# Kernel tuning notes

Hardware: AMD Instinct MI355X
Metric: run time of the kernel (lower is better)

Reference implementation:

```python
import jax, jax.numpy as jnp
import numpy as np

B = 1024
N_NODES = 30
E_PER = 82
IN_F = 128
HID = 256
HEADS = (3, 2, 1)
N_EH = 41


def _lin(k, fi, fo):
    s = 1.0 / np.sqrt(fi)
    kw, kb = jax.random.split(k)
    W = jax.random.uniform(kw, (fi, fo), jnp.float32, -s, s)
    b = jax.random.uniform(kb, (fo,), jnp.float32, -s, s)
    return W, b


def setup_inputs() -> dict:
    key = jax.random.key(0)
    ks = list(jax.random.split(key, 32))
    rng = np.random.default_rng(0)
    # base 30-node graph with E_PER directed edges, no self-loops
    src = rng.integers(0, N_NODES, E_PER)
    dst = (src + rng.integers(1, N_NODES, E_PER)) % N_NODES
    base = np.stack([src, dst])  # [2, E_PER]
    offs = (np.arange(B) * N_NODES)[None, None, :]  # [1,1,B]
    ei = (base[:, :, None] + offs).transpose(0, 2, 1).reshape(2, -1)  # [2, B*E_PER]
    e_h = rng.choice(E_PER, N_EH, replace=False)
    d = {}
    d["x"] = jax.random.normal(ks[0], (B * N_NODES, IN_F), jnp.float32)
    d["edge_index"] = jnp.asarray(ei, dtype=jnp.int32)
    d["e_h_pairs"] = jnp.asarray(base[:, e_h].T, dtype=jnp.int32)  # [N_EH, 2]
    d["Wp"], d["bp"] = _lin(ks[1], IN_F, HID)
    i = 2
    for l, H in enumerate(HEADS):
        d[f"ln_g{l}"] = jnp.ones((HID,), jnp.float32)
        d[f"ln_b{l}"] = jnp.zeros((HID,), jnp.float32)
        d[f"Wl{l}"], d[f"bl{l}"] = _lin(ks[i], HID, H * HID); i += 1
        d[f"Wr{l}"], d[f"br{l}"] = _lin(ks[i], HID, H * HID); i += 1
        d[f"att{l}"] = jax.random.normal(ks[i], (H, HID), jnp.float32) * 0.1; i += 1
        d[f"bias{l}"] = jnp.zeros((HID,), jnp.float32)
    dims = [2 * HID, 256, 128, 128, 1]
    for j in range(4):
        d[f"Wm{j}"], d[f"bm{j}"] = _lin(ks[i], dims[j], dims[j + 1]); i += 1
    return d


def _layer_norm(h, g, b):
    mu = jnp.mean(h, -1, keepdims=True)
    var = jnp.mean((h - mu) ** 2, -1, keepdims=True)
    return (h - mu) * jax.lax.rsqrt(var + 1e-5) * g + b


def _gatv2(h, src, dst, n, Wl, bl, Wr, br, att, bias):
    # PyG GATv2Conv, concat=False (mean over heads), self-loops already in src/dst
    H, C = att.shape
    xl = (h @ Wl + bl).reshape(-1, H, C)  # source transform
    xr = (h @ Wr + br).reshape(-1, H, C)  # target transform
    xj = xl[src]                          # [E,H,C]
    e = jax.nn.leaky_relu(xj + xr[dst], 0.2)
    logits = jnp.einsum('ehc,hc->eh', e, att)  # [E,H]
    m = jax.lax.stop_gradient(jax.ops.segment_max(logits, dst, num_segments=n))
    ex = jnp.exp(logits - m[dst])
    denom = jax.ops.segment_sum(ex, dst, num_segments=n)
    alpha = ex / denom[dst]               # softmax over incoming edges of dst
    out = jax.ops.segment_sum(xj * alpha[..., None], dst, num_segments=n)  # [N,H,C]
    return jnp.mean(out, 1) + bias


def reference(x, edge_index, e_h_pairs, Wp, bp,
              ln_g0, ln_b0, Wl0, bl0, Wr0, br0, att0, bias0,
              ln_g1, ln_b1, Wl1, bl1, Wr1, br1, att1, bias1,
              ln_g2, ln_b2, Wl2, bl2, Wr2, br2, att2, bias2,
              Wm0, bm0, Wm1, bm1, Wm2, bm2, Wm3, bm3):
    n = x.shape[0]
    loops = jnp.arange(n, dtype=edge_index.dtype)
    src = jnp.concatenate([edge_index[0], loops])
    dst = jnp.concatenate([edge_index[1], loops])
    lrelu = lambda v: jax.nn.leaky_relu(v, 0.01)
    h = x @ Wp + bp
    layers = [(ln_g0, ln_b0, Wl0, bl0, Wr0, br0, att0, bias0),
              (ln_g1, ln_b1, Wl1, bl1, Wr1, br1, att1, bias1),
              (ln_g2, ln_b2, Wl2, bl2, Wr2, br2, att2, bias2)]
    for (g, b, Wl, bl, Wr, br, att, bias) in layers:
        hn = _layer_norm(h, g, b)
        hc = _gatv2(hn, src, dst, n, Wl, bl, Wr, br, att, bias)
        h = lrelu(hc) + h  # dropout is identity in eval
    hb = h.reshape(-1, N_NODES, HID)  # [B, 30, 256]
    ef = jnp.concatenate([hb[:, e_h_pairs[:, 0], :], hb[:, e_h_pairs[:, 1], :]], -1)
    o = ef.reshape(-1, 2 * HID)
    o = lrelu(o @ Wm0 + bm0)
    o = lrelu(o @ Wm1 + bm1)
    o = lrelu(o @ Wm2 + bm2)
    o = o @ Wm3 + bm3
    return o.reshape(-1)
```

## Files before the change

kernel.cpp:

```cpp
#include <hip/hip_runtime.h>
#include <hip/hip_bf16.h>
#include <math.h>

#define N_NODES 30
#define E_BASE  82
#define E_TOT   112
#define B_GRAPH 1024
#define HID     256
#define NTOT    (B_GRAPH * N_NODES)
#define MAXIN   32
#define N_EH    41
#define M_MLP   (B_GRAPH * N_EH)

#define META_SRC  0
#define META_DST  E_TOT
#define META_CNT  (2 * E_TOT)
#define META_LIST 256
#define META_INTS 1216

typedef __attribute__((ext_vector_type(8))) short bf16x8;
typedef __attribute__((ext_vector_type(4))) short bf16x4;
typedef __attribute__((ext_vector_type(4))) float f32x4;
#define AS3 __attribute__((address_space(3)))
#define AS1 __attribute__((address_space(1)))
// ... 25 lines not shown
      if (tid < E_BASE) { s = ei[tid]; d = ei[B_GRAPH * E_BASE + tid]; }
      else              { s = tid - E_BASE; d = s; }
      meta[META_SRC + tid] = s;
      meta[META_DST + tid] = d;
      int pos = atomicAdd(&cnt[d], 1);
      if (pos < MAXIN) meta[META_LIST + d * MAXIN + pos] = tid;
    }
    __syncthreads();
    if (tid < N_NODES) meta[META_CNT + tid] = cnt[tid];
    return;
  }
  int ji = 0;
  #pragma unroll
  for (int i = 1; i < 10; i++) if (b >= args.j[i].tstart) ji = i;
  WtJob jb = args.j[ji];
  int t = b - jb.tstart;
  int ntn = jb.N >> 5;
  int tk = t / ntn, tn = t - tk * ntn;
  int k0 = tk * 32, n0 = tn * 32;
  __shared__ float s[32][33];
  int tx = threadIdx.x & 31, ty = threadIdx.x >> 5;
  #pragma unroll
  for (int p = 0; p < 4; p++)
    s[ty + p * 8][tx] = jb.in[(size_t)(k0 + ty + p * 8) * jb.N + n0 + tx];
  __syncthreads();
  __hip_bfloat16* o = out + jb.ooff;
  #pragma unroll
  for (int p = 0; p < 4; p++) {
    int n = ty + p * 8;
    o[(size_t)(n0 + n) * jb.K + k0 + tx] = __float2bfloat16(s[tx][n]);
  }
}

template<int ACT, int OUTBF>
__global__ __launch_bounds__(256)
void gemm_mfma(const __hip_bfloat16* __restrict__ A, const __hip_bfloat16* __restrict__ Bt,
               const float* __restrict__ bias, const float* __restrict__ bias2,
               void* __restrict__ Cv, int M, int K, int N, int N1)
{
  __shared__ __hip_bfloat16 sA[2][128 * 32];
  __shared__ __hip_bfloat16 sB[2][128 * 32];
  const int tid = threadIdx.x;
  const int lane = tid & 63;
  const int wave = tid >> 6;
  const int wx = wave & 1, wy = wave >> 1;
  const int bm = blockIdx.x, bn = blockIdx.y;
  const int mrow = lane & 15, quad = lane >> 4;

  const int r0 = tid >> 2, kc0 = (tid & 3) * 8;
  const __hip_bfloat16* Ag0 = A + (size_t)(bm * 128 + r0) * K + kc0;
  const __hip_bfloat16* Ag1 = A + (size_t)(bm * 128 + r0 + 64) * K + kc0;
  const __hip_bfloat16* Bg0 = Bt + (size_t)(bn * 128 + r0) * K + kc0;
  const __hip_bfloat16* Bg1 = Bt + (size_t)(bn * 128 + r0 + 64) * K + kc0;

  f32x4 acc[4][4];
  #pragma unroll
  for (int i = 0; i < 4; i++)
    #pragma unroll
    for (int j = 0; j < 4; j++)
      acc[i][j] = (f32x4){0.f, 0.f, 0.f, 0.f};

  for (int kt = 0; kt < K; kt += 64) {
    __syncthreads();
    #pragma unroll
    for (int s = 0; s < 2; s++) {
      gload_lds16(Ag0 + kt + s * 32, &sA[s][tid * 8]);
      gload_lds16(Ag1 + kt + s * 32, &sA[s][2048 + tid * 8]);
      gload_lds16(Bg0 + kt + s * 32, &sB[s][tid * 8]);
      gload_lds16(Bg1 + kt + s * 32, &sB[s][2048 + tid * 8]);
    }
    __syncthreads();

    #pragma unroll
    for (int s = 0; s < 2; s++) {
      bf16x8 af[4], bfr[4];
      #pragma unroll
      for (int i = 0; i < 4; i++) {
        af[i]  = *(const bf16x8*)&sA[s][(wy * 64 + i * 16 + mrow) * 32 + quad * 8];
        bfr[i] = *(const bf16x8*)&sB[s][(wx * 64 + i * 16 + mrow) * 32 + quad * 8];
      }
      #pragma unroll
      for (int i = 0; i < 4; i++)
        #pragma unroll
        for (int j = 0; j < 4; j++)
          acc[i][j] = __builtin_amdgcn_mfma_f32_16x16x32_bf16(af[i], bfr[j], acc[i][j], 0, 0, 0);
    }
  }

  #pragma unroll
  for (int i = 0; i < 4; i++) {
    #pragma unroll
    for (int r = 0; r < 4; r++) {
      size_t row = (size_t)bm * 128 + wy * 64 + i * 16 + quad * 4 + r;
      #pragma unroll
      for (int j = 0; j < 4; j++) {
        int col = bn * 128 + wx * 64 + j * 16 + mrow;
        float bc = (col < N1) ? bias[col] : bias2[col - N1];
        float v = acc[i][j][r] + bc;
        if (ACT) v = v > 0.f ? v : 0.01f * v;
        if (OUTBF) ((__hip_bfloat16*)Cv)[row * N + col] = __float2bfloat16(v);
        else       ((float*)Cv)[row * N + col] = v;
      }
    }
  }
}

template<int ACT, int OUTBF>
__global__ __launch_bounds__(256)
void gemm_mfma_f32a(const float* __restrict__ A, const __hip_bfloat16* __restrict__ Bt,
                    const float* __restrict__ bias, void* __restrict__ Cv,
                    int M, int K, int N)
{
  __shared__ __hip_bfloat16 sA[128 * 32];
  __shared__ __hip_bfloat16 sB[128 * 32];
  const int tid = threadIdx.x;
  const int lane = tid & 63;
  const int wave = tid >> 6;
  const int wx = wave & 1, wy = wave >> 1;
  const int bm = blockIdx.x, bn = blockIdx.y;
  const int mrow = lane & 15, quad = lane >> 4;

  const int r0 = tid >> 2, kc0 = (tid & 3) * 8;
  const float* Ag0 = A + (size_t)(bm * 128 + r0) * K + kc0;
  const float* Ag1 = A + (size_t)(bm * 128 + r0 + 64) * K + kc0;
  const __hip_bfloat16* Bg0 = Bt + (size_t)(bn * 128 + r0) * K + kc0;
  const __hip_bfloat16* Bg1 = Bt + (size_t)(bn * 128 + r0 + 64) * K + kc0;

  f32x4 acc[4][4];
  #pragma unroll
  for (int i = 0; i < 4; i++)
    #pragma unroll
    for (int j = 0; j < 4; j++)
      acc[i][j] = (f32x4){0.f, 0.f, 0.f, 0.f};

// ... 58 lines not shown
  const int K = 512;
  __shared__ __hip_bfloat16 sA[128 * 32];
  __shared__ __hip_bfloat16 sB[128 * 32];
  const int tid = threadIdx.x;
  const int lane = tid & 63;
  const int wave = tid >> 6;
  const int wx = wave & 1, wy = wave >> 1;
  const int bm = blockIdx.x, bn = blockIdx.y;
  const int mrow = lane & 15, quad = lane >> 4;

  const float* pu[2]; const float* pv[2]; int sub[2];
  #pragma unroll
  for (int cI = 0; cI < 2; cI++) {
    int c = tid + cI * 256;
    int r0 = c >> 2; sub[cI] = (c & 3) * 8;
    int R = bm * 128 + r0;
    int b = R / N_EH, p = R - b * N_EH;
    int u = pairs[p * 2], v = pairs[p * 2 + 1];
    pu[cI] = h + ((size_t)b * N_NODES + u) * HID;
    pv[cI] = h + ((size_t)b * N_NODES + v) * HID;
  }

  const int r0 = tid >> 2, kc0 = (tid & 3) * 8;
  const __hip_bfloat16* Bg0 = Bt + (size_t)(bn * 128 + r0) * K + kc0;
  const __hip_bfloat16* Bg1 = Bt + (size_t)(bn * 128 + r0 + 64) * K + kc0;

  f32x4 acc[4][4];
  #pragma unroll
  for (int i = 0; i < 4; i++)
    #pragma unroll
    for (int j = 0; j < 4; j++)
      acc[i][j] = (f32x4){0.f, 0.f, 0.f, 0.f};

  for (int kt = 0; kt < K; kt += 32) {
    float4 av[2][2];
    #pragma unroll
    for (int cI = 0; cI < 2; cI++) {
      const float* src = (kt < 256 ? pu[cI] + kt : pv[cI] + kt - 256) + sub[cI];
      av[cI][0] = *(const float4*)src;
      av[cI][1] = *(const float4*)(src + 4);
    }
    __syncthreads();
    #pragma unroll
    for (int cI = 0; cI < 2; cI++) {
      __hip_bfloat16 t[8];
      t[0] = __float2bfloat16(av[cI][0].x); t[1] = __float2bfloat16(av[cI][0].y);
      t[2] = __float2bfloat16(av[cI][0].z); t[3] = __float2bfloat16(av[cI][0].w);
      t[4] = __float2bfloat16(av[cI][1].x); t[5] = __float2bfloat16(av[cI][1].y);
      t[6] = __float2bfloat16(av[cI][1].z); t[7] = __float2bfloat16(av[cI][1].w);
      *(bf16x8*)&sA[(tid + cI * 256) * 8] = *(bf16x8*)t;
    }
    gload_lds16(Bg0 + kt, &sB[tid * 8]);
    gload_lds16(Bg1 + kt, &sB[2048 + tid * 8]);
    __syncthreads();

    bf16x8 af[4], bfr[4];
    #pragma unroll
    for (int i = 0; i < 4; i++) {
      af[i]  = *(const bf16x8*)&sA[(wy * 64 + i * 16 + mrow) * 32 + quad * 8];
      bfr[i] = *(const bf16x8*)&sB[(wx * 64 + i * 16 + mrow) * 32 + quad * 8];
    }
    #pragma unroll
    for (int i = 0; i < 4; i++)
      #pragma unroll
      for (int j = 0; j < 4; j++)
        acc[i][j] = __builtin_amdgcn_mfma_f32_16x16x32_bf16(af[i], bfr[j], acc[i][j], 0, 0, 0);
  }
// ... 134 lines not shown
      }
    }
  }
  __syncthreads();
  if (tid < 128)
    out[(size_t)bm * 128 + tid] = spart[0][tid] + spart[1][tid] + b3[0];
}

__global__ __launch_bounds__(256)
void layernorm(const float* __restrict__ h, const float* __restrict__ g,
               const float* __restrict__ b, __hip_bfloat16* __restrict__ hn)
{
  const int wv = threadIdx.x >> 6, lane = threadIdx.x & 63;
  const size_t row = (size_t)blockIdx.x * 4 + wv;
  const float* hr = h + row * HID;
  float v[4];
  float sum = 0.f;
  #pragma unroll
  for (int j = 0; j < 4; j++) { v[j] = hr[lane + 64 * j]; sum += v[j]; }
  #pragma unroll
  for (int off = 32; off; off >>= 1) sum += __shfl_xor(sum, off);
  float mu = sum * (1.f / 256.f);
  float vs = 0.f;
  #pragma unroll
  for (int j = 0; j < 4; j++) { float d = v[j] - mu; vs += d * d; }
  #pragma unroll
  for (int off = 32; off; off >>= 1) vs += __shfl_xor(vs, off);
  float rs = rsqrtf(vs * (1.f / 256.f) + 1e-5f);
  __hip_bfloat16* outr = hn + row * HID;
  #pragma unroll
  for (int j = 0; j < 4; j++) {
    int c = lane + 64 * j;
    outr[c] = __float2bfloat16((v[j] - mu) * rs * g[c] + b[c]);
  }
}

__global__ __launch_bounds__(256)
void gat_alpha(const __hip_bfloat16* __restrict__ xcat,
               const float* __restrict__ att, float* __restrict__ alphaG,
               const int* __restrict__ meta, int H)
{
  __shared__ __hip_bfloat16 sxl[N_NODES * HID];
  __shared__ __hip_bfloat16 sxr[N_NODES * HID];
  __shared__ float slog[E_TOT];
  __shared__ float smax[N_NODES];
  __shared__ float sden[N_NODES];
  __shared__ int ssrc[E_TOT], sdst[E_TOT], scnt[N_NODES], slist[N_NODES * MAXIN];

  const int tid = threadIdx.x;
  const int g = blockIdx.x, hh = blockIdx.y;
  const size_t nodebase = (size_t)g * N_NODES;
  const int S = 2 * H * HID;

  {
    int i = tid;
    #pragma unroll
    for (int p = 0; p < 4; p++, i += 256) {
      if (i < N_NODES * HID / 8) {
        int node = i >> 5, c = (i & 31) * 8;
        const __hip_bfloat16* row = &xcat[(nodebase + node) * S + c];
        gload_lds16(row + hh * HID, &sxl[(size_t)i * 8]);
        gload_lds16(row + (H + hh) * HID, &sxr[(size_t)i * 8]);
      }
    }
  }

  if (tid < E_TOT) { ssrc[tid] = meta[META_SRC + tid]; sdst[tid] = meta[META_DST + tid]; }
  if (tid < N_NODES) { scnt[tid] = meta[META_CNT + tid]; sden[tid] = 0.f; }
  for (int i = tid; i < N_NODES * MAXIN; i += 256) slist[i] = meta[META_LIST + i];

  const int wv = tid >> 6, l32 = tid & 31, esub = (tid >> 5) & 1;
  const int c0 = l32 * 8;
  float attr[8];
  #pragma unroll
  for (int j = 0; j < 8; j++) attr[j] = att[hh * HID + c0 + j];
  __syncthreads();

  #pragma unroll
  for (int pass = 0; pass < 14; pass++) {
    int e = pass * 8 + wv * 2 + esub;
    bf16x8 a = *(const bf16x8*)&sxl[ssrc[e] * HID + c0];
    bf16x8 b = *(const bf16x8*)&sxr[sdst[e] * HID + c0];
    float sum = 0.f;
    #pragma unroll
    for (int j = 0; j < 8; j++) {
      float v = b2f(a[j]) + b2f(b[j]);
      v = v > 0.f ? v : 0.2f * v;
      sum += v * attr[j];
    }
    #pragma unroll
    for (int off = 16; off; off >>= 1) sum += __shfl_xor(sum, off);
    if (l32 == 0) slog[e] = sum;
  }
  __syncthreads();

  if (tid < N_NODES) {
    int cnt = scnt[tid];
    const int* lst = &slist[tid * MAXIN];
    float m = -1e30f;
    for (int i = 0; i < cnt; i++) m = fmaxf(m, slog[lst[i]]);
    smax[tid] = m;
  }
  __syncthreads();
  if (tid < E_TOT) {
    float ex = expf(slog[tid] - smax[sdst[tid]]);
    slog[tid] = ex;
    atomicAdd(&sden[sdst[tid]], ex);
  }
  __syncthreads();
  if (tid < E_TOT)
    alphaG[((size_t)g * H + hh) * E_TOT + tid] = slog[tid] / sden[sdst[tid]];
}

template<int DO_LN>
__global__ __launch_bounds__(256, 4)
void gat_agg(const __hip_bfloat16* __restrict__ xcat, const float* __restrict__ alphaG,
             const float* __restrict__ bias, float* __restrict__ h,
             const float* __restrict__ lnG, const float* __restrict__ lnB,
             __hip_bfloat16* __restrict__ hn, const int* __restrict__ meta, int H)
{
  __shared__ __hip_bfloat16 sxl[2][N_NODES * HID];
  __shared__ float salpha[2][E_TOT];
  __shared__ int ssrc[E_TOT], scnt[N_NODES], slist[N_NODES * MAXIN];

  const int tid = threadIdx.x;
  const int g = blockIdx.x;
  const size_t nodebase = (size_t)g * N_NODES;
  const int S = 2 * H * HID;
  const int c4 = tid & 63;
  const int ng = tid >> 6;

  if (tid < E_TOT) ssrc[tid] = meta[META_SRC + tid];
  if (tid < N_NODES) scnt[tid] = meta[META_CNT + tid];
  for (int i = tid; i < N_NODES * MAXIN; i += 256) slist[i] = meta[META_LIST + i];

  float4 hres[8];
  #pragma unroll
  for (int ki = 0; ki < 8; ki++) {
    int k = ng + ki * 4;
    if (k < N_NODES) hres[ki] = *(const float4*)&h[(nodebase + k) * HID + c4 * 4];
  }

  {
    int i = tid;
    #pragma unroll
    for (int p = 0; p < 4; p++, i += 256) {
      if (i < N_NODES * HID / 8) {
        int node = i >> 5, c = (i & 31) * 8;
        gload_lds16(&xcat[(nodebase + node) * S + 0 * HID + c], &sxl[0][(size_t)i * 8]);
      }
    }
    if (tid < E_TOT) salpha[0][tid] = alphaG[((size_t)g * H + 0) * E_TOT + tid];
  }

  float acc[8][4];
  #pragma unroll
  for (int ki = 0; ki < 8; ki++)
    #pragma unroll
    for (int j = 0; j < 4; j++) acc[ki][j] = 0.f;

  for (int hh = 0; hh < H; hh++) {
    const int buf = hh & 1;
    __syncthreads();
    if (hh + 1 < H) {
      const int nb = buf ^ 1;
      int i = tid;
      #pragma unroll
      for (int p = 0; p < 4; p++, i += 256) {
        if (i < N_NODES * HID / 8) {
          int node = i >> 5, c = (i & 31) * 8;
          gload_lds16(&xcat[(nodebase + node) * S + (hh + 1) * HID + c], &sxl[nb][(size_t)i * 8]);
        }
      }
      if (tid < E_TOT) salpha[nb][tid] = alphaG[((size_t)g * H + hh + 1) * E_TOT + tid];
    }
    #pragma unroll
    for (int ki = 0; ki < 8; ki++) {
      int k = ng + ki * 4;
      if (k < N_NODES) {
        int cnt = scnt[k];
        const int* lst = &slist[k * MAXIN];
        for (int i = 0; i < cnt; i++) {
          int e = lst[i];
          float al = salpha[buf][e];
          bf16x4 v = *(const bf16x4*)&sxl[buf][ssrc[e] * HID + c4 * 4];
          acc[ki][0] += al * b2f(v[0]);
          acc[ki][1] += al * b2f(v[1]);
          acc[ki][2] += al * b2f(v[2]);
          acc[ki][3] += al * b2f(v[3]);
        }
      }
    }
  }

  const float invH = 1.f / (float)H;
  const float4 bs = *(const float4*)&bias[c4 * 4];
  float4 gv, bv;
  if (DO_LN) {
    gv = *(const float4*)&lnG[c4 * 4];
    bv = *(const float4*)&lnB[c4 * 4];
  }
  #pragma unroll
  for (int ki = 0; ki < 8; ki++) {
    int k = ng + ki * 4;
    if (k < N_NODES) {
      float o0 = acc[ki][0] * invH + bs.x; o0 = o0 > 0.f ? o0 : 0.01f * o0; o0 += hres[ki].x;
      float o1 = acc[ki][1] * invH + bs.y; o1 = o1 > 0.f ? o1 : 0.01f * o1; o1 += hres[ki].y;
      float o2 = acc[ki][2] * invH + bs.z; o2 = o2 > 0.f ? o2 : 0.01f * o2; o2 += hres[ki].z;
      float o3 = acc[ki][3] * invH + bs.w; o3 = o3 > 0.f ? o3 : 0.01f * o3; o3 += hres[ki].w;
      float4 o4 = {o0, o1, o2, o3};
      *(float4*)&h[(nodebase + k) * HID + c4 * 4] = o4;
      if (DO_LN) {
        float sum = o0 + o1 + o2 + o3;
        #pragma unroll
        for (int off = 32; off; off >>= 1) sum += __shfl_xor(sum, off);
        float mu = sum * (1.f / 256.f);
        float d0 = o0 - mu, d1 = o1 - mu, d2 = o2 - mu, d3 = o3 - mu;
        float vs = d0 * d0 + d1 * d1 + d2 * d2 + d3 * d3;
        #pragma unroll
        for (int off = 32; off; off >>= 1) vs += __shfl_xor(vs, off);
        float rs = rsqrtf(vs * (1.f / 256.f) + 1e-5f);
        __hip_bfloat16 t[4];
        t[0] = __float2bfloat16(d0 * rs * gv.x + bv.x);
        t[1] = __float2bfloat16(d1 * rs * gv.y + bv.y);
        t[2] = __float2bfloat16(d2 * rs * gv.z + bv.z);
        t[3] = __float2bfloat16(d3 * rs * gv.w + bv.w);
        *(bf16x4*)&hn[(nodebase + k) * HID + c4 * 4] = *(bf16x4*)t;
      }
    }
  }
}

extern "C" void kernel_launch(void* const* d_in, const int* in_sizes, int n_in,
                              void* d_out, int out_size, void* d_ws, size_t ws_size,
                              hipStream_t stream) {
  const float* x     = (const float*)d_in[0];
  const int*   ei    = (const int*)d_in[1];
  const int*   pairs = (const int*)d_in[2];
  const float* bp    = (const float*)d_in[4];
  const float *lng[3], *lnb[3], *bl[3], *br[3], *att[3], *bias[3];
  const float *WlF[3], *WrF[3];
  for (int l = 0; l < 3; l++) {
    int base = 5 + l * 8;
    lng[l]  = (const float*)d_in[base + 0];
    lnb[l]  = (const float*)d_in[base + 1];
    WlF[l]  = (const float*)d_in[base + 2];
    bl[l]   = (const float*)d_in[base + 3];
    WrF[l]  = (const float*)d_in[base + 4];
    br[l]   = (const float*)d_in[base + 5];
    att[l]  = (const float*)d_in[base + 6];
    bias[l] = (const float*)d_in[base + 7];
  }
  const float* WmF[4] = {(const float*)d_in[29], (const float*)d_in[31],
                         (const float*)d_in[33], (const float*)d_in[35]};
  const float* bm[4] = {(const float*)d_in[30], (const float*)d_in[32],
                        (const float*)d_in[34], (const float*)d_in[36]};

  float* ws  = (float*)d_ws;
  float* h   = ws;
  __hip_bfloat16* hnb = (__hip_bfloat16*)(ws + 7864320);
  __hip_bfloat16* xcat = (__hip_bfloat16*)(ws + 11796480);
  float* alphaG = ws + 35389440;
  __hip_bfloat16* wbuf = (__hip_bfloat16*)(ws + 35733504);
  int*   meta = (int*)(ws + 36233216);
  __hip_bfloat16* o1b = (__hip_bfloat16*)xcat;
  float* out = (float*)d_out;

  const int oWp = 0, oWl0 = 32768, oWr0 = 229376, oWl1 = 425984, oWr1 = 557056;
  const int oWl2 = 688128, oWr2 = 753664, oWm0 = 819200, oWm1 = 950272, oWm2 = 983040;

  WtArgs wa;
  wa.j[0] = {(const float*)d_in[3], 128, 256,   0, oWp };
  wa.j[1] = {WlF[0],              256, 768,  32, oWl0};
  wa.j[2] = {WrF[0],              256, 768, 224, oWr0};
  wa.j[3] = {WlF[1],              256, 512, 416, oWl1};
  wa.j[4] = {WrF[1],              256, 512, 544, oWr1};
  wa.j[5] = {WlF[2],              256, 256, 672, oWl2};
  wa.j[6] = {WrF[2],              256, 256, 736, oWr2};
  wa.j[7] = {WmF[0],              512, 256, 800, oWm0};
  wa.j[8] = {WmF[1],              256, 128, 928, oWm1};
  wa.j[9] = {WmF[2],              128, 128, 960, oWm2};
  transpose_weights<<<977, 256, 0, stream>>>(wa, wbuf, ei, meta);

  gemm_mfma_f32a<0, 0><<<dim3(NTOT / 128, 2), 256, 0, stream>>>(x, wbuf + oWp, bp, h,
                                                                NTOT, 128, 256);

  layernorm<<<NTOT / 4, 256, 0, stream>>>(h, lng[0], lnb[0], hnb);

  const int Hs[3] = {3, 2, 1};
  const int oWl[3] = {oWl0, oWl1, oWl2};
  for (int l = 0; l < 3; l++) {
    int N = 2 * Hs[l] * HID;
    gemm_mfma<0, 1><<<dim3(NTOT / 128, N / 128), 256, 0, stream>>>(
        hnb, wbuf + oWl[l], bl[l], br[l], xcat, NTOT, HID, N, N / 2);
    gat_alpha<<<dim3(B_GRAPH, Hs[l]), 256, 0, stream>>>(xcat, att[l], alphaG, meta, Hs[l]);
    if (l < 2)
      gat_agg<1><<<B_GRAPH, 256, 0, stream>>>(xcat, alphaG, bias[l], h,
                                              lng[l + 1], lnb[l + 1], hnb, meta, Hs[l]);
    else
      gat_agg<0><<<B_GRAPH, 256, 0, stream>>>(xcat, alphaG, bias[l], h,
                                              nullptr, nullptr, nullptr, meta, Hs[l]);
  }

  gemm_mfma_pair<<<dim3(M_MLP / 128, 2), 256, 0, stream>>>(h, pairs, wbuf + oWm0, bm[0], o1b, 256);
  mlp_tail<<<M_MLP / 128, 256, 0, stream>>>(o1b, wbuf + oWm1, bm[1], wbuf + oWm2, bm[2],
                                            WmF[3], bm[3], out);
}
```

Before: 437.5 us.

## Fuse GATv2 projection GEMM, attention and aggregation into one per-graph kernel

Replaces the per-layer sequence of projection GEMM, attention-logit kernel and aggregation kernel with a single kernel per layer, where each block owns one 30-node graph. The block computes the xl/xr projections with MFMA into shared memory and runs softmax and aggregation in place. This removes the large bf16 xcat intermediate and the alpha buffer round trips through global memory, and cuts launches from 9 to 3. In exchange, weights are read directly from global memory per block with no LDS tiling. The GEMM works on 32-row tiles padded from 30 rows, and the larger LDS footprint may lower occupancy.

```diff
diff --git a/kernel.cpp b/kernel.cpp
--- a/kernel.cpp
+++ b/kernel.cpp
@@ -81,74 +81,202 @@
   }
 }
 
-template<int ACT, int OUTBF>
+template<int DO_LN>
 __global__ __launch_bounds__(256)
-void gemm_mfma(const __hip_bfloat16* __restrict__ A, const __hip_bfloat16* __restrict__ Bt,
-               const float* __restrict__ bias, const float* __restrict__ bias2,
-               void* __restrict__ Cv, int M, int K, int N, int N1)
+void gat_fused(const __hip_bfloat16* hnb_io,
+               const __hip_bfloat16* __restrict__ Wl,
+               const __hip_bfloat16* __restrict__ Wr,
+               const float* __restrict__ blv, const float* __restrict__ brv,
+               const float* __restrict__ att, const float* __restrict__ bias,
+               float* __restrict__ h,
+               const float* __restrict__ lnG, const float* __restrict__ lnB,
+               const int* __restrict__ meta, int H)
 {
-  __shared__ __hip_bfloat16 sA[2][128 * 32];
-  __shared__ __hip_bfloat16 sB[2][128 * 32];
+  __shared__ __hip_bfloat16 sHn[8 * 32 * 32];
+  __shared__ __hip_bfloat16 sxl[N_NODES * HID];
+  __shared__ __hip_bfloat16 sxr[N_NODES * HID];
+  __shared__ float slog[E_TOT], salpha[E_TOT], smax[N_NODES], sden[N_NODES];
+  __shared__ int ssrc[E_TOT], sdst[E_TOT], scnt[N_NODES], slist[N_NODES * MAXIN];
+
   const int tid = threadIdx.x;
-  const int lane = tid & 63;
-  const int wave = tid >> 6;
-  const int wx = wave & 1, wy = wave >> 1;
-  const int bm = blockIdx.x, bn = blockIdx.y;
+  const int g = blockIdx.x;
+  const size_t nodebase = (size_t)g * N_NODES;
+  const int lane = tid & 63, wave = tid >> 6;
   const int mrow = lane & 15, quad = lane >> 4;
-
-  const int r0 = tid >> 2, kc0 = (tid & 3) * 8;
-  const __hip_bfloat16* Ag0 = A + (size_t)(bm * 128 + r0) * K + kc0;
-  const __hip_bfloat16* Ag1 = A + (size_t)(bm * 128 + r0 + 64) * K + kc0;
-  const __hip_bfloat16* Bg0 = Bt + (size_t)(bn * 128 + r0) * K + kc0;
-  const __hip_bfloat16* Bg1 = Bt + (size_t)(bn * 128 + r0 + 64) * K + kc0;
-
-  f32x4 acc[4][4];
-  #pragma unroll
-  for (int i = 0; i < 4; i++)
-    #pragma unroll
-    for (int j = 0; j < 4; j++)
-      acc[i][j] = (f32x4){0.f, 0.f, 0.f, 0.f};
-
-  for (int kt = 0; kt < K; kt += 64) {
-    __syncthreads();
-    #pragma unroll
-    for (int s = 0; s < 2; s++) {
-      gload_lds16(Ag0 + kt + s * 32, &sA[s][tid * 8]);
-      gload_lds16(Ag1 + kt + s * 32, &sA[s][2048 + tid * 8]);
-      gload_lds16(Bg0 + kt + s * 32, &sB[s][tid * 8]);
-      gload_lds16(Bg1 + kt + s * 32, &sB[s][2048 + tid * 8]);
-    }
-    __syncthreads();
-
-    #pragma unroll
-    for (int s = 0; s < 2; s++) {
-      bf16x8 af[4], bfr[4];
-      #pragma unroll
-      for (int i = 0; i < 4; i++) {
-        af[i]  = *(const bf16x8*)&sA[s][(wy * 64 + i * 16 + mrow) * 32 + quad * 8];
-        bfr[i] = *(const bf16x8*)&sB[s][(wx * 64 + i * 16 + mrow) * 32 + quad * 8];
-      }
-      #pragma unroll
-      for (int i = 0; i < 4; i++)
-        #pragma unroll
-        for (int j = 0; j < 4; j++)
-          acc[i][j] = __builtin_amdgcn_mfma_f32_16x16x32_bf16(af[i], bfr[j], acc[i][j], 0, 0, 0);
-    }
-  }
-
-  #pragma unroll
-  for (int i = 0; i < 4; i++) {
-    #pragma unroll
-    for (int r = 0; r < 4; r++) {
-      size_t row = (size_t)bm * 128 + wy * 64 + i * 16 + quad * 4 + r;
-      #pragma unroll
-      for (int j = 0; j < 4; j++) {
-        int col = bn * 128 + wx * 64 + j * 16 + mrow;
-        float bc = (col < N1) ? bias[col] : bias2[col - N1];
-        float v = acc[i][j][r] + bc;
-        if (ACT) v = v > 0.f ? v : 0.01f * v;
-        if (OUTBF) ((__hip_bfloat16*)Cv)[row * N + col] = __float2bfloat16(v);
-        else       ((float*)Cv)[row * N + col] = v;
+  const int n0 = wave * 64;
+  const int c4 = tid & 63, ng = tid >> 6;
+
+  {
+    const __hip_bfloat16* src = hnb_io + nodebase * HID;
+    #pragma unroll
+    for (int p = 0; p < 4; p++) {
+      int L = tid + p * 256;
+      int kk = L >> 7, rem = L & 127;
+      int row = rem >> 2, c16 = rem & 3;
+      if (row >= N_NODES) row = 0;
+      gload_lds16(src + (size_t)(row * 32 + kk * 4 + c16) * 8, &sHn[(size_t)L * 8]);
+    }
+  }
+  if (tid < E_TOT) { ssrc[tid] = meta[META_SRC + tid]; sdst[tid] = meta[META_DST + tid]; }
+  if (tid < N_NODES) scnt[tid] = meta[META_CNT + tid];
+  for (int i = tid; i < N_NODES * MAXIN; i += 256) slist[i] = meta[META_LIST + i];
+  __syncthreads();
+
+  float agg[8][4];
+  #pragma unroll
+  for (int ki = 0; ki < 8; ki++)
+    #pragma unroll
+    for (int j = 0; j < 4; j++) agg[ki][j] = 0.f;
+
+  for (int hh = 0; hh < H; hh++) {
+    for (int mat = 0; mat < 2; mat++) {
+      const __hip_bfloat16* W = (mat ? Wr : Wl) + ((size_t)hh * HID) * HID;
+      const float* bb = mat ? brv : blv;
+      __hip_bfloat16* sx = mat ? sxr : sxl;
+
+      f32x4 acc[2][4];
+      #pragma unroll
+      for (int mi = 0; mi < 2; mi++)
+        #pragma unroll
+        for (int nj = 0; nj < 4; nj++) acc[mi][nj] = (f32x4){0.f, 0.f, 0.f, 0.f};
+
+      #pragma unroll
+      for (int kk = 0; kk < 8; kk++) {
+        bf16x8 a0 = *(const bf16x8*)&sHn[kk * 1024 + mrow * 32 + quad * 8];
+        bf16x8 a1 = *(const bf16x8*)&sHn[kk * 1024 + (16 + mrow) * 32 + quad * 8];
+        bf16x8 bf[4];
+        #pragma unroll
+        for (int nj = 0; nj < 4; nj++)
+          bf[nj] = *(const bf16x8*)&W[(size_t)(n0 + nj * 16 + mrow) * HID + kk * 32 + quad * 8];
+        #pragma unroll
+        for (int nj = 0; nj < 4; nj++) {
+          acc[0][nj] = __builtin_amdgcn_mfma_f32_16x16x32_bf16(a0, bf[nj], acc[0][nj], 0, 0, 0);
+          acc[1][nj] = __builtin_amdgcn_mfma_f32_16x16x32_bf16(a1, bf[nj], acc[1][nj], 0, 0, 0);
+        }
+      }
+
+      if (mat == 0) __syncthreads();
+
+      float bv[4];
+      #pragma unroll
+      for (int nj = 0; nj < 4; nj++) bv[nj] = bb[hh * HID + n0 + nj * 16 + mrow];
+      #pragma unroll
+      for (int mi = 0; mi < 2; mi++) {
+        #pragma unroll
+        for (int r = 0; r < 4; r++) {
+          int row = mi * 16 + quad * 4 + r;
+          if (row < N_NODES) {
+            #pragma unroll
+            for (int nj = 0; nj < 4; nj++)
+              sx[row * HID + n0 + nj * 16 + mrow] = __float2bfloat16(acc[mi][nj][r] + bv[nj]);
+          }
+        }
+      }
+    }
+    __syncthreads();
+
+    {
+      const int l32 = tid & 31, esub = (tid >> 5) & 1;
+      const int c0 = l32 * 8;
+      float attr[8];
+      #pragma unroll
+      for (int j = 0; j < 8; j++) attr[j] = att[hh * HID + c0 + j];
+      if (tid < N_NODES) sden[tid] = 0.f;
+      #pragma unroll
+      for (int pass = 0; pass < 14; pass++) {
+        int e = pass * 8 + wave * 2 + esub;
+        bf16x8 a = *(const bf16x8*)&sxl[ssrc[e] * HID + c0];
+        bf16x8 b = *(const bf16x8*)&sxr[sdst[e] * HID + c0];
+        float sum = 0.f;
+        #pragma unroll
+        for (int j = 0; j < 8; j++) {
+          float v = b2f(a[j]) + b2f(b[j]);
+          v = v > 0.f ? v : 0.2f * v;
+          sum += v * attr[j];
+        }
+        #pragma unroll
+        for (int off = 16; off; off >>= 1) sum += __shfl_xor(sum, off);
+        if (l32 == 0) slog[e] = sum;
+      }
+    }
+    __syncthreads();
+
+    if (tid < N_NODES) {
+      int cnt = scnt[tid];
+      const int* lst = &slist[tid * MAXIN];
+      float m = -1e30f;
+      for (int i = 0; i < cnt; i++) m = fmaxf(m, slog[lst[i]]);
+      smax[tid] = m;
+    }
+    __syncthreads();
+    if (tid < E_TOT) {
+      float ex = expf(slog[tid] - smax[sdst[tid]]);
+      slog[tid] = ex;
+      atomicAdd(&sden[sdst[tid]], ex);
+    }
+    __syncthreads();
+    if (tid < E_TOT) salpha[tid] = slog[tid] / sden[sdst[tid]];
+    __syncthreads();
+
+    #pragma unroll
+    for (int ki = 0; ki < 8; ki++) {
+      int k = ng + ki * 4;
+      if (k < N_NODES) {
+        int cnt = scnt[k];
+        const int* lst = &slist[k * MAXIN];
+        for (int i = 0; i < cnt; i++) {
+          int e = lst[i];
+          float al = salpha[e];
+          bf16x4 v = *(const bf16x4*)&sxl[ssrc[e] * HID + c4 * 4];
+          agg[ki][0] += al * b2f(v[0]);
+          agg[ki][1] += al * b2f(v[1]);
+          agg[ki][2] += al * b2f(v[2]);
+          agg[ki][3] += al * b2f(v[3]);
+        }
+      }
+    }
+  }
+
+  float4 hres[8];
+  #pragma unroll
+  for (int ki = 0; ki < 8; ki++) {
+    int k = ng + ki * 4;
+    if (k < N_NODES) hres[ki] = *(const float4*)&h[(nodebase + k) * HID + c4 * 4];
+  }
+  const float invH = 1.f / (float)H;
+  const float4 bs = *(const float4*)&bias[c4 * 4];
+  float4 gv, bv;
+  if (DO_LN) {
+    gv = *(const float4*)&lnG[c4 * 4];
+    bv = *(const float4*)&lnB[c4 * 4];
+  }
+  __hip_bfloat16* hn_out = (__hip_bfloat16*)hnb_io;
+  #pragma unroll
+  for (int ki = 0; ki < 8; ki++) {
+    int k = ng + ki * 4;
+    if (k < N_NODES) {
+      float o0 = agg[ki][0] * invH + bs.x; o0 = o0 > 0.f ? o0 : 0.01f * o0; o0 += hres[ki].x;
+      float o1 = agg[ki][1] * invH + bs.y; o1 = o1 > 0.f ? o1 : 0.01f * o1; o1 += hres[ki].y;
+      float o2 = agg[ki][2] * invH + bs.z; o2 = o2 > 0.f ? o2 : 0.01f * o2; o2 += hres[ki].z;
+      float o3 = agg[ki][3] * invH + bs.w; o3 = o3 > 0.f ? o3 : 0.01f * o3; o3 += hres[ki].w;
+      float4 o4 = {o0, o1, o2, o3};
+      *(float4*)&h[(nodebase + k) * HID + c4 * 4] = o4;
+      if (DO_LN) {
+        float sum = o0 + o1 + o2 + o3;
+        #pragma unroll
+        for (int off = 32; off; off >>= 1) sum += __shfl_xor(sum, off);
+        float mu = sum * (1.f / 256.f);
+        float d0 = o0 - mu, d1 = o1 - mu, d2 = o2 - mu, d3 = o3 - mu;
+        float vs = d0 * d0 + d1 * d1 + d2 * d2 + d3 * d3;
+        #pragma unroll
+        for (int off = 32; off; off >>= 1) vs += __shfl_xor(vs, off);
+        float rs = rsqrtf(vs * (1.f / 256.f) + 1e-5f);
+        __hip_bfloat16 t[4];
+        t[0] = __float2bfloat16(d0 * rs * gv.x + bv.x);
+        t[1] = __float2bfloat16(d1 * rs * gv.y + bv.y);
+        t[2] = __float2bfloat16(d2 * rs * gv.z + bv.z);
+        t[3] = __float2bfloat16(d3 * rs * gv.w + bv.w);
+        *(bf16x4*)&hn_out[(nodebase + k) * HID + c4 * 4] = *(bf16x4*)t;
       }
     }
   }
@@ -474,202 +602,6 @@
   for (int j = 0; j < 4; j++) {
     int c = lane + 64 * j;
     outr[c] = __float2bfloat16((v[j] - mu) * rs * g[c] + b[c]);
-  }
-}
-
-__global__ __launch_bounds__(256)
-void gat_alpha(const __hip_bfloat16* __restrict__ xcat,
-               const float* __restrict__ att, float* __restrict__ alphaG,
-               const int* __restrict__ meta, int H)
-{
-  __shared__ __hip_bfloat16 sxl[N_NODES * HID];
-  __shared__ __hip_bfloat16 sxr[N_NODES * HID];
-  __shared__ float slog[E_TOT];
-  __shared__ float smax[N_NODES];
-  __shared__ float sden[N_NODES];
-  __shared__ int ssrc[E_TOT], sdst[E_TOT], scnt[N_NODES], slist[N_NODES * MAXIN];
-
-  const int tid = threadIdx.x;
-  const int g = blockIdx.x, hh = blockIdx.y;
-  const size_t nodebase = (size_t)g * N_NODES;
-  const int S = 2 * H * HID;
-
-  {
-    int i = tid;
-    #pragma unroll
-    for (int p = 0; p < 4; p++, i += 256) {
-      if (i < N_NODES * HID / 8) {
-        int node = i >> 5, c = (i & 31) * 8;
-        const __hip_bfloat16* row = &xcat[(nodebase + node) * S + c];
-        gload_lds16(row + hh * HID, &sxl[(size_t)i * 8]);
-        gload_lds16(row + (H + hh) * HID, &sxr[(size_t)i * 8]);
-      }
-    }
-  }
-
-  if (tid < E_TOT) { ssrc[tid] = meta[META_SRC + tid]; sdst[tid] = meta[META_DST + tid]; }
-  if (tid < N_NODES) { scnt[tid] = meta[META_CNT + tid]; sden[tid] = 0.f; }
-  for (int i = tid; i < N_NODES * MAXIN; i += 256) slist[i] = meta[META_LIST + i];
-
-  const int wv = tid >> 6, l32 = tid & 31, esub = (tid >> 5) & 1;
-  const int c0 = l32 * 8;
-  float attr[8];
-  #pragma unroll
-  for (int j = 0; j < 8; j++) attr[j] = att[hh * HID + c0 + j];
-  __syncthreads();
-
-  #pragma unroll
-  for (int pass = 0; pass < 14; pass++) {
-    int e = pass * 8 + wv * 2 + esub;
-    bf16x8 a = *(const bf16x8*)&sxl[ssrc[e] * HID + c0];
-    bf16x8 b = *(const bf16x8*)&sxr[sdst[e] * HID + c0];
-    float sum = 0.f;
-    #pragma unroll
-    for (int j = 0; j < 8; j++) {
-      float v = b2f(a[j]) + b2f(b[j]);
-      v = v > 0.f ? v : 0.2f * v;
-      sum += v * attr[j];
-    }
-    #pragma unroll
-    for (int off = 16; off; off >>= 1) sum += __shfl_xor(sum, off);
-    if (l32 == 0) slog[e] = sum;
-  }
-  __syncthreads();
-
-  if (tid < N_NODES) {
-    int cnt = scnt[tid];
-    const int* lst = &slist[tid * MAXIN];
-    float m = -1e30f;
-    for (int i = 0; i < cnt; i++) m = fmaxf(m, slog[lst[i]]);
-    smax[tid] = m;
-  }
-  __syncthreads();
-  if (tid < E_TOT) {
-    float ex = expf(slog[tid] - smax[sdst[tid]]);
-    slog[tid] = ex;
-    atomicAdd(&sden[sdst[tid]], ex);
-  }
-  __syncthreads();
-  if (tid < E_TOT)
-    alphaG[((size_t)g * H + hh) * E_TOT + tid] = slog[tid] / sden[sdst[tid]];
-}
-
-template<int DO_LN>
-__global__ __launch_bounds__(256, 4)
-void gat_agg(const __hip_bfloat16* __restrict__ xcat, const float* __restrict__ alphaG,
-             const float* __restrict__ bias, float* __restrict__ h,
-             const float* __restrict__ lnG, const float* __restrict__ lnB,
-             __hip_bfloat16* __restrict__ hn, const int* __restrict__ meta, int H)
-{
-  __shared__ __hip_bfloat16 sxl[2][N_NODES * HID];
-  __shared__ float salpha[2][E_TOT];
-  __shared__ int ssrc[E_TOT], scnt[N_NODES], slist[N_NODES * MAXIN];
-
-  const int tid = threadIdx.x;
-  const int g = blockIdx.x;
-  const size_t nodebase = (size_t)g * N_NODES;
-  const int S = 2 * H * HID;
-  const int c4 = tid & 63;
-  const int ng = tid >> 6;
-
-  if (tid < E_TOT) ssrc[tid] = meta[META_SRC + tid];
-  if (tid < N_NODES) scnt[tid] = meta[META_CNT + tid];
-  for (int i = tid; i < N_NODES * MAXIN; i += 256) slist[i] = meta[META_LIST + i];
-
-  float4 hres[8];
-  #pragma unroll
-  for (int ki = 0; ki < 8; ki++) {
-    int k = ng + ki * 4;
-    if (k < N_NODES) hres[ki] = *(const float4*)&h[(nodebase + k) * HID + c4 * 4];
-  }
-
-  {
-    int i = tid;
-    #pragma unroll
-    for (int p = 0; p < 4; p++, i += 256) {
-      if (i < N_NODES * HID / 8) {
-        int node = i >> 5, c = (i & 31) * 8;
-        gload_lds16(&xcat[(nodebase + node) * S + 0 * HID + c], &sxl[0][(size_t)i * 8]);
-      }
-    }
-    if (tid < E_TOT) salpha[0][tid] = alphaG[((size_t)g * H + 0) * E_TOT + tid];
-  }
-
-  float acc[8][4];
-  #pragma unroll
-  for (int ki = 0; ki < 8; ki++)
-    #pragma unroll
-    for (int j = 0; j < 4; j++) acc[ki][j] = 0.f;
-
-  for (int hh = 0; hh < H; hh++) {
-    const int buf = hh & 1;
-    __syncthreads();
-    if (hh + 1 < H) {
-      const int nb = buf ^ 1;
-      int i = tid;
-      #pragma unroll
-      for (int p = 0; p < 4; p++, i += 256) {
-        if (i < N_NODES * HID / 8) {
-          int node = i >> 5, c = (i & 31) * 8;
-          gload_lds16(&xcat[(nodebase + node) * S + (hh + 1) * HID + c], &sxl[nb][(size_t)i * 8]);
-        }
-      }
-      if (tid < E_TOT) salpha[nb][tid] = alphaG[((size_t)g * H + hh + 1) * E_TOT + tid];
-    }
-    #pragma unroll
-    for (int ki = 0; ki < 8; ki++) {
-      int k = ng + ki * 4;
-      if (k < N_NODES) {
-        int cnt = scnt[k];
-        const int* lst = &slist[k * MAXIN];
-        for (int i = 0; i < cnt; i++) {
-          int e = lst[i];
-          float al = salpha[buf][e];
-          bf16x4 v = *(const bf16x4*)&sxl[buf][ssrc[e] * HID + c4 * 4];
-          acc[ki][0] += al * b2f(v[0]);
-          acc[ki][1] += al * b2f(v[1]);
-          acc[ki][2] += al * b2f(v[2]);
-          acc[ki][3] += al * b2f(v[3]);
-        }
-      }
-    }
-  }
-
-  const float invH = 1.f / (float)H;
-  const float4 bs = *(const float4*)&bias[c4 * 4];
-  float4 gv, bv;
-  if (DO_LN) {
-    gv = *(const float4*)&lnG[c4 * 4];
-    bv = *(const float4*)&lnB[c4 * 4];
-  }
-  #pragma unroll
-  for (int ki = 0; ki < 8; ki++) {
-    int k = ng + ki * 4;
-    if (k < N_NODES) {
-      float o0 = acc[ki][0] * invH + bs.x; o0 = o0 > 0.f ? o0 : 0.01f * o0; o0 += hres[ki].x;
-      float o1 = acc[ki][1] * invH + bs.y; o1 = o1 > 0.f ? o1 : 0.01f * o1; o1 += hres[ki].y;
-      float o2 = acc[ki][2] * invH + bs.z; o2 = o2 > 0.f ? o2 : 0.01f * o2; o2 += hres[ki].z;
-      float o3 = acc[ki][3] * invH + bs.w; o3 = o3 > 0.f ? o3 : 0.01f * o3; o3 += hres[ki].w;
-      float4 o4 = {o0, o1, o2, o3};
-      *(float4*)&h[(nodebase + k) * HID + c4 * 4] = o4;
-      if (DO_LN) {
-        float sum = o0 + o1 + o2 + o3;
-        #pragma unroll
-        for (int off = 32; off; off >>= 1) sum += __shfl_xor(sum, off);
-        float mu = sum * (1.f / 256.f);
-        float d0 = o0 - mu, d1 = o1 - mu, d2 = o2 - mu, d3 = o3 - mu;
-        float vs = d0 * d0 + d1 * d1 + d2 * d2 + d3 * d3;
-        #pragma unroll
-        for (int off = 32; off; off >>= 1) vs += __shfl_xor(vs, off);
-        float rs = rsqrtf(vs * (1.f / 256.f) + 1e-5f);
-        __hip_bfloat16 t[4];
-        t[0] = __float2bfloat16(d0 * rs * gv.x + bv.x);
-        t[1] = __float2bfloat16(d1 * rs * gv.y + bv.y);
-        t[2] = __float2bfloat16(d2 * rs * gv.z + bv.z);
-        t[3] = __float2bfloat16(d3 * rs * gv.w + bv.w);
-        *(bf16x4*)&hn[(nodebase + k) * HID + c4 * 4] = *(bf16x4*)t;
-      }
-    }
   }
 }
 
@@ -701,11 +633,9 @@
   float* ws  = (float*)d_ws;
   float* h   = ws;
   __hip_bfloat16* hnb = (__hip_bfloat16*)(ws + 7864320);
-  __hip_bfloat16* xcat = (__hip_bfloat16*)(ws + 11796480);
-  float* alphaG = ws + 35389440;
+  __hip_bfloat16* o1b = (__hip_bfloat16*)(ws + 11796480);
   __hip_bfloat16* wbuf = (__hip_bfloat16*)(ws + 35733504);
   int*   meta = (int*)(ws + 36233216);
-  __hip_bfloat16* o1b = (__hip_bfloat16*)xcat;
   float* out = (float*)d_out;
 
   const int oWp = 0, oWl0 = 32768, oWr0 = 229376, oWl1 = 425984, oWr1 = 557056;
@@ -729,20 +659,12 @@
 
   layernorm<<<NTOT / 4, 256, 0, stream>>>(h, lng[0], lnb[0], hnb);
 
-  const int Hs[3] = {3, 2, 1};
-  const int oWl[3] = {oWl0, oWl1, oWl2};
-  for (int l = 0; l < 3; l++) {
-    int N = 2 * Hs[l] * HID;
-    gemm_mfma<0, 1><<<dim3(NTOT / 128, N / 128), 256, 0, stream>>>(
-        hnb, wbuf + oWl[l], bl[l], br[l], xcat, NTOT, HID, N, N / 2);
-    gat_alpha<<<dim3(B_GRAPH, Hs[l]), 256, 0, stream>>>(xcat, att[l], alphaG, meta, Hs[l]);
-    if (l < 2)
-      gat_agg<1><<<B_GRAPH, 256, 0, stream>>>(xcat, alphaG, bias[l], h,
-                                              lng[l + 1], lnb[l + 1], hnb, meta, Hs[l]);
-    else
-      gat_agg<0><<<B_GRAPH, 256, 0, stream>>>(xcat, alphaG, bias[l], h,
-                                              nullptr, nullptr, nullptr, meta, Hs[l]);
-  }
+  gat_fused<1><<<B_GRAPH, 256, 0, stream>>>(hnb, wbuf + oWl0, wbuf + oWr0, bl[0], br[0],
+                                            att[0], bias[0], h, lng[1], lnb[1], meta, 3);
+  gat_fused<1><<<B_GRAPH, 256, 0, stream>>>(hnb, wbuf + oWl1, wbuf + oWr1, bl[1], br[1],
+                                            att[1], bias[1], h, lng[2], lnb[2], meta, 2);
+  gat_fused<0><<<B_GRAPH, 256, 0, stream>>>(hnb, wbuf + oWl2, wbuf + oWr2, bl[2], br[2],
+                                            att[2], bias[2], h, nullptr, nullptr, meta, 1);
 
   gemm_mfma_pair<<<dim3(M_MLP / 128, 2), 256, 0, stream>>>(h, pairs, wbuf + oWm0, bm[0], o1b, 256);
   mlp_tail<<<M_MLP / 128, 256, 0, stream>>>(o1b, wbuf + oWm1, bm[1], wbuf + oWm2, bm[2],
```

Result: slower. 537.7 us (+22.9%).

## Fuse GATv2 attention-softmax kernel into aggregation kernel per graph

Applied to the files above, without the earlier changes.

Merges the separate gat_alpha kernel into the aggregation kernel, so each block computes the attention logits, softmax and weighted aggregation for all heads of one graph. This removes the alphaG round trip through global memory, one kernel launch per layer, and the second read of xl rows. The cost is extra shared memory for the xr buffer, lower occupancy (launch bounds 3 instead of 4) and more barriers inside the head loop. It also hardcodes the pair-GEMM K loop bound to 512.

```diff
diff --git a/kernel.cpp b/kernel.cpp
--- a/kernel.cpp
+++ b/kernel.cpp
@@ -273,7 +273,7 @@
     for (int j = 0; j < 4; j++)
       acc[i][j] = (f32x4){0.f, 0.f, 0.f, 0.f};
 
-  for (int kt = 0; kt < K; kt += 32) {
+  for (int kt = 0; kt < 512; kt += 32) {
     float4 av[2][2];
     #pragma unroll
     for (int cI = 0; cI < 2; cI++) {
@@ -477,93 +477,17 @@
   }
 }
 
-__global__ __launch_bounds__(256)
-void gat_alpha(const __hip_bfloat16* __restrict__ xcat,
-               const float* __restrict__ att, float* __restrict__ alphaG,
-               const int* __restrict__ meta, int H)
-{
-  __shared__ __hip_bfloat16 sxl[N_NODES * HID];
-  __shared__ __hip_bfloat16 sxr[N_NODES * HID];
-  __shared__ float slog[E_TOT];
-  __shared__ float smax[N_NODES];
-  __shared__ float sden[N_NODES];
-  __shared__ int ssrc[E_TOT], sdst[E_TOT], scnt[N_NODES], slist[N_NODES * MAXIN];
-
-  const int tid = threadIdx.x;
-  const int g = blockIdx.x, hh = blockIdx.y;
-  const size_t nodebase = (size_t)g * N_NODES;
-  const int S = 2 * H * HID;
-
-  {
-    int i = tid;
-    #pragma unroll
-    for (int p = 0; p < 4; p++, i += 256) {
-      if (i < N_NODES * HID / 8) {
-        int node = i >> 5, c = (i & 31) * 8;
-        const __hip_bfloat16* row = &xcat[(nodebase + node) * S + c];
-        gload_lds16(row + hh * HID, &sxl[(size_t)i * 8]);
-        gload_lds16(row + (H + hh) * HID, &sxr[(size_t)i * 8]);
-      }
-    }
-  }
-
-  if (tid < E_TOT) { ssrc[tid] = meta[META_SRC + tid]; sdst[tid] = meta[META_DST + tid]; }
-  if (tid < N_NODES) { scnt[tid] = meta[META_CNT + tid]; sden[tid] = 0.f; }
-  for (int i = tid; i < N_NODES * MAXIN; i += 256) slist[i] = meta[META_LIST + i];
-
-  const int wv = tid >> 6, l32 = tid & 31, esub = (tid >> 5) & 1;
-  const int c0 = l32 * 8;
-  float attr[8];
-  #pragma unroll
-  for (int j = 0; j < 8; j++) attr[j] = att[hh * HID + c0 + j];
-  __syncthreads();
-
-  #pragma unroll
-  for (int pass = 0; pass < 14; pass++) {
-    int e = pass * 8 + wv * 2 + esub;
-    bf16x8 a = *(const bf16x8*)&sxl[ssrc[e] * HID + c0];
-    bf16x8 b = *(const bf16x8*)&sxr[sdst[e] * HID + c0];
-    float sum = 0.f;
-    #pragma unroll
-    for (int j = 0; j < 8; j++) {
-      float v = b2f(a[j]) + b2f(b[j]);
-      v = v > 0.f ? v : 0.2f * v;
-      sum += v * attr[j];
-    }
-    #pragma unroll
-    for (int off = 16; off; off >>= 1) sum += __shfl_xor(sum, off);
-    if (l32 == 0) slog[e] = sum;
-  }
-  __syncthreads();
-
-  if (tid < N_NODES) {
-    int cnt = scnt[tid];
-    const int* lst = &slist[tid * MAXIN];
-    float m = -1e30f;
-    for (int i = 0; i < cnt; i++) m = fmaxf(m, slog[lst[i]]);
-    smax[tid] = m;
-  }
-  __syncthreads();
-  if (tid < E_TOT) {
-    float ex = expf(slog[tid] - smax[sdst[tid]]);
-    slog[tid] = ex;
-    atomicAdd(&sden[sdst[tid]], ex);
-  }
-  __syncthreads();
-  if (tid < E_TOT)
-    alphaG[((size_t)g * H + hh) * E_TOT + tid] = slog[tid] / sden[sdst[tid]];
-}
-
 template<int DO_LN>
-__global__ __launch_bounds__(256, 4)
-void gat_agg(const __hip_bfloat16* __restrict__ xcat, const float* __restrict__ alphaG,
-             const float* __restrict__ bias, float* __restrict__ h,
-             const float* __restrict__ lnG, const float* __restrict__ lnB,
-             __hip_bfloat16* __restrict__ hn, const int* __restrict__ meta, int H)
+__global__ __launch_bounds__(256, 3)
+void gat_alag(const __hip_bfloat16* __restrict__ xcat, const float* __restrict__ att,
+              const float* __restrict__ bias, float* __restrict__ h,
+              const float* __restrict__ lnG, const float* __restrict__ lnB,
+              __hip_bfloat16* __restrict__ hn, const int* __restrict__ meta, int H)
 {
   __shared__ __hip_bfloat16 sxl[2][N_NODES * HID];
-  __shared__ float salpha[2][E_TOT];
-  __shared__ int ssrc[E_TOT], scnt[N_NODES], slist[N_NODES * MAXIN];
+  __shared__ __hip_bfloat16 sxr[N_NODES * HID];
+  __shared__ float slog[E_TOT], salpha[E_TOT], smax[N_NODES], sden[N_NODES];
+  __shared__ int ssrc[E_TOT], sdst[E_TOT], scnt[N_NODES], slist[N_NODES * MAXIN];
 
   const int tid = threadIdx.x;
   const int g = blockIdx.x;
@@ -571,8 +495,9 @@
   const int S = 2 * H * HID;
   const int c4 = tid & 63;
   const int ng = tid >> 6;
-
-  if (tid < E_TOT) ssrc[tid] = meta[META_SRC + tid];
+  const int wv = tid >> 6;
+
+  if (tid < E_TOT) { ssrc[tid] = meta[META_SRC + tid]; sdst[tid] = meta[META_DST + tid]; }
   if (tid < N_NODES) scnt[tid] = meta[META_CNT + tid];
   for (int i = tid; i < N_NODES * MAXIN; i += 256) slist[i] = meta[META_LIST + i];
 
@@ -589,33 +514,90 @@
     for (int p = 0; p < 4; p++, i += 256) {
       if (i < N_NODES * HID / 8) {
         int node = i >> 5, c = (i & 31) * 8;
-        gload_lds16(&xcat[(nodebase + node) * S + 0 * HID + c], &sxl[0][(size_t)i * 8]);
-      }
-    }
-    if (tid < E_TOT) salpha[0][tid] = alphaG[((size_t)g * H + 0) * E_TOT + tid];
-  }
-
-  float acc[8][4];
+        const __hip_bfloat16* row = &xcat[(nodebase + node) * S + c];
+        gload_lds16(row + 0 * HID, &sxl[0][(size_t)i * 8]);
+        gload_lds16(row + H * HID, &sxr[(size_t)i * 8]);
+      }
+    }
+  }
+
+  float agg[8][4];
   #pragma unroll
   for (int ki = 0; ki < 8; ki++)
     #pragma unroll
-    for (int j = 0; j < 4; j++) acc[ki][j] = 0.f;
+    for (int j = 0; j < 4; j++) agg[ki][j] = 0.f;
 
   for (int hh = 0; hh < H; hh++) {
     const int buf = hh & 1;
     __syncthreads();
+
     if (hh + 1 < H) {
-      const int nb = buf ^ 1;
       int i = tid;
       #pragma unroll
       for (int p = 0; p < 4; p++, i += 256) {
         if (i < N_NODES * HID / 8) {
           int node = i >> 5, c = (i & 31) * 8;
-          gload_lds16(&xcat[(nodebase + node) * S + (hh + 1) * HID + c], &sxl[nb][(size_t)i * 8]);
+          gload_lds16(&xcat[(nodebase + node) * S + (hh + 1) * HID + c],
+                      &sxl[buf ^ 1][(size_t)i * 8]);
         }
       }
-      if (tid < E_TOT) salpha[nb][tid] = alphaG[((size_t)g * H + hh + 1) * E_TOT + tid];
-    }
+    }
+
+    if (tid < N_NODES) sden[tid] = 0.f;
+    {
+      const int l32 = tid & 31, esub = (tid >> 5) & 1;
+      const int c0 = l32 * 8;
+      float attr[8];
+      #pragma unroll
+      for (int j = 0; j < 8; j++) attr[j] = att[hh * HID + c0 + j];
+      #pragma unroll
+      for (int pass = 0; pass < 14; pass++) {
+        int e = pass * 8 + wv * 2 + esub;
+        bf16x8 a = *(const bf16x8*)&sxl[buf][ssrc[e] * HID + c0];
+        bf16x8 b = *(const bf16x8*)&sxr[sdst[e] * HID + c0];
+        float sum = 0.f;
+        #pragma unroll
+        for (int j = 0; j < 8; j++) {
+          float v = b2f(a[j]) + b2f(b[j]);
+          v = v > 0.f ? v : 0.2f * v;
+          sum += v * attr[j];
+        }
+        #pragma unroll
+        for (int off = 16; off; off >>= 1) sum += __shfl_xor(sum, off);
+        if (l32 == 0) slog[e] = sum;
+      }
+    }
+    __syncthreads();
+
+    if (hh + 1 < H) {
+      int i = tid;
+      #pragma unroll
+      for (int p = 0; p < 4; p++, i += 256) {
+        if (i < N_NODES * HID / 8) {
+          int node = i >> 5, c = (i & 31) * 8;
+          gload_lds16(&xcat[(nodebase + node) * S + (H + hh + 1) * HID + c],
+                      &sxr[(size_t)i * 8]);
+        }
+      }
+    }
+
+    if (tid < N_NODES) {
+      int cnt = scnt[tid];
+      const int* lst = &slist[tid * MAXIN];
+      float m = -1e30f;
+      for (int i = 0; i < cnt; i++) m = fmaxf(m, slog[lst[i]]);
+      smax[tid] = m;
+    }
+    __syncthreads();
+    if (tid < E_TOT) {
+      float ex = expf(slog[tid] - smax[sdst[tid]]);
+      slog[tid] = ex;
+      atomicAdd(&sden[sdst[tid]], ex);
+    }
+    __syncthreads();
+    if (tid < E_TOT) salpha[tid] = slog[tid] / sden[sdst[tid]];
+    __syncthreads();
+
     #pragma unroll
     for (int ki = 0; ki < 8; ki++) {
       int k = ng + ki * 4;
@@ -624,12 +606,12 @@
         const int* lst = &slist[k * MAXIN];
         for (int i = 0; i < cnt; i++) {
           int e = lst[i];
-          float al = salpha[buf][e];
+          float al = salpha[e];
           bf16x4 v = *(const bf16x4*)&sxl[buf][ssrc[e] * HID + c4 * 4];
-          acc[ki][0] += al * b2f(v[0]);
-          acc[ki][1] += al * b2f(v[1]);
-          acc[ki][2] += al * b2f(v[2]);
-          acc[ki][3] += al * b2f(v[3]);
+          agg[ki][0] += al * b2f(v[0]);
+          agg[ki][1] += al * b2f(v[1]);
+          agg[ki][2] += al * b2f(v[2]);
+          agg[ki][3] += al * b2f(v[3]);
         }
       }
     }
@@ -646,10 +628,10 @@
   for (int ki = 0; ki < 8; ki++) {
     int k = ng + ki * 4;
     if (k < N_NODES) {
-      float o0 = acc[ki][0] * invH + bs.x; o0 = o0 > 0.f ? o0 : 0.01f * o0; o0 += hres[ki].x;
-      float o1 = acc[ki][1] * invH + bs.y; o1 = o1 > 0.f ? o1 : 0.01f * o1; o1 += hres[ki].y;
-      float o2 = acc[ki][2] * invH + bs.z; o2 = o2 > 0.f ? o2 : 0.01f * o2; o2 += hres[ki].z;
-      float o3 = acc[ki][3] * invH + bs.w; o3 = o3 > 0.f ? o3 : 0.01f * o3; o3 += hres[ki].w;
+      float o0 = agg[ki][0] * invH + bs.x; o0 = o0 > 0.f ? o0 : 0.01f * o0; o0 += hres[ki].x;
+      float o1 = agg[ki][1] * invH + bs.y; o1 = o1 > 0.f ? o1 : 0.01f * o1; o1 += hres[ki].y;
+      float o2 = agg[ki][2] * invH + bs.z; o2 = o2 > 0.f ? o2 : 0.01f * o2; o2 += hres[ki].z;
+      float o3 = agg[ki][3] * invH + bs.w; o3 = o3 > 0.f ? o3 : 0.01f * o3; o3 += hres[ki].w;
       float4 o4 = {o0, o1, o2, o3};
       *(float4*)&h[(nodebase + k) * HID + c4 * 4] = o4;
       if (DO_LN) {
@@ -702,7 +684,6 @@
   float* h   = ws;
   __hip_bfloat16* hnb = (__hip_bfloat16*)(ws + 7864320);
   __hip_bfloat16* xcat = (__hip_bfloat16*)(ws + 11796480);
-  float* alphaG = ws + 35389440;
   __hip_bfloat16* wbuf = (__hip_bfloat16*)(ws + 35733504);
   int*   meta = (int*)(ws + 36233216);
   __hip_bfloat16* o1b = (__hip_bfloat16*)xcat;
@@ -735,13 +716,12 @@
     int N = 2 * Hs[l] * HID;
     gemm_mfma<0, 1><<<dim3(NTOT / 128, N / 128), 256, 0, stream>>>(
         hnb, wbuf + oWl[l], bl[l], br[l], xcat, NTOT, HID, N, N / 2);
-    gat_alpha<<<dim3(B_GRAPH, Hs[l]), 256, 0, stream>>>(xcat, att[l], alphaG, meta, Hs[l]);
     if (l < 2)
-      gat_agg<1><<<B_GRAPH, 256, 0, stream>>>(xcat, alphaG, bias[l], h,
-                                              lng[l + 1], lnb[l + 1], hnb, meta, Hs[l]);
+      gat_alag<1><<<B_GRAPH, 256, 0, stream>>>(xcat, att[l], bias[l], h,
+                                               lng[l + 1], lnb[l + 1], hnb, meta, Hs[l]);
     else
-      gat_agg<0><<<B_GRAPH, 256, 0, stream>>>(xcat, alphaG, bias[l], h,
-                                              nullptr, nullptr, nullptr, meta, Hs[l]);
+      gat_alag<0><<<B_GRAPH, 256, 0, stream>>>(xcat, att[l], bias[l], h,
+                                               nullptr, nullptr, nullptr, meta, Hs[l]);
   }
 
   gemm_mfma_pair<<<dim3(M_MLP / 128, 2), 256, 0, stream>>>(h, pairs, wbuf + oWm0, bm[0], o1b, 256);
```

Measured after the change: 472.8 us. 1.08x slower.
